# Kernel tuning notes

Hardware: AMD Instinct MI355X
Metric: run time of the kernel (lower is better)

## Reference

```python
import jax, jax.numpy as jnp
import numpy as np

B, S, D, H = 4, 2048, 1024, 16
HD = D // H  # 64


def setup_inputs() -> dict:
    key = jax.random.key(0)
    ks = jax.random.split(key, 4)
    scale = 0.02
    return {
        "hidden_states": jax.random.normal(ks[0], (B, S, D), dtype=jnp.float32),
        "pad": jnp.ones((B, S), dtype=jnp.float32),  # 1 = keep, 0 = pad
        "wq": jax.random.normal(ks[1], (D, D), dtype=jnp.float32) * scale,
        "bq": jnp.zeros((D,), dtype=jnp.float32),
        "wk": jax.random.normal(ks[2], (D, D), dtype=jnp.float32) * scale,
        "bk": jnp.zeros((D,), dtype=jnp.float32),
        "wv": jax.random.normal(ks[3], (D, D), dtype=jnp.float32) * scale,
        "bv": jnp.zeros((D,), dtype=jnp.float32),
    }


def reference(hidden_states, pad, wq, bq, wk, bk, wv, bv):
    # QKV projections (torch Linear: x @ W^T + b); weights stored as [out, in]
    q = hidden_states @ wq.T + bq  # [B,S,D]
    k = hidden_states @ wk.T + bk
    v = hidden_states @ wv.T + bv

    def split_heads(x):
        return x.reshape(B, S, H, HD).transpose(0, 2, 1, 3)  # [B,H,S,HD]

    q, k, v = split_heads(q), split_heads(k), split_heads(v)

    score = jnp.einsum("bhqd,bhkd->bhqk", q, k) / jnp.sqrt(jnp.float32(HD))
    # additive pad mask: (1 - pad) * -1e9, broadcast over heads and query dim
    mask_bias = (1.0 - pad)[:, None, None, :] * (-1e9)
    prob = jax.nn.softmax(score + mask_bias, axis=-1)  # [B,H,S,S]

    context = jnp.einsum("bhqk,bhkd->bhqd", prob, v)  # [B,H,S,HD]
    context = context.transpose(0, 2, 1, 3).reshape(B, S, D)
    return context
```

## Files before the change

kernel.cpp:

```cpp
#include <hip/hip_runtime.h>
#include <cstdint>
#include <cstddef>

#define B_ 4
#define S_ 2048
#define D_ 1024
#define H_ 16

typedef unsigned short u16;
typedef unsigned int u32;
typedef __attribute__((ext_vector_type(8))) short bf16x8;
typedef __attribute__((ext_vector_type(4))) float f32x4;

__device__ __forceinline__ u16 f2bf(float f) {
  union { float f; u32 u; } x; x.f = f;
  u32 r = x.u + 0x7fffu + ((x.u >> 16) & 1u);
  return (u16)(r >> 16);
}

__device__ __forceinline__ u32 cvtpk_bf16(float lo, float hi) {
  u32 r;
  asm("v_cvt_pk_bf16_f32 %0, %1, %2" : "=v"(r) : "v"(lo), "v"(hi));
  return r;
}

__device__ __forceinline__ float max3f(float a, float b, float c) {
  return fmaxf(fmaxf(a, b), c);
}

__device__ __forceinline__ f32x4 mfma16(bf16x8 a, bf16x8 b, f32x4 c) {
  return __builtin_amdgcn_mfma_f32_16x16x32_bf16(a, b, c, 0, 0, 0);
}

__device__ __forceinline__ void gload_lds16(const u16* g, u16* l) {
  __builtin_amdgcn_global_load_lds((const __attribute__((address_space(1))) void*)g,
                                   (__attribute__((address_space(3))) void*)l,
                                   16, 0, 0);
}

__global__ __launch_bounds__(256) void cvt_kernel(const float4* __restrict__ src,
                                                  uint2* __restrict__ dst, int n4) {
  int i = blockIdx.x * 256 + threadIdx.x;
  if (i < n4) {
    float4 v = src[i];
    uint2 o;
    o.x = cvtpk_bf16(v.x, v.y);
    o.y = cvtpk_bf16(v.z, v.w);
    dst[i] = o;
  }
}

__global__ __launch_bounds__(256) void qkv_gemm(
    const u16* __restrict__ A, const u16* __restrict__ Bm,
    const float* __restrict__ bq, const float* __restrict__ bk,
    const float* __restrict__ bv,
    u16* __restrict__ qbuf, u16* __restrict__ kbuf, u16* __restrict__ vtbuf)
{
  __shared__ __align__(16) u16 lA[128 * 64];
  __shared__ __align__(16) u16 lB[128 * 64];

  const int bid = blockIdx.x;
  const int wg = ((bid & 7) * 192) + (bid >> 3);
  const int bm = wg & 63;
  const int bn = wg >> 6;
  const int tid = threadIdx.x;
  const int wid = tid >> 6, lane = tid & 63;
  const int g = lane >> 4, c = lane & 15;
  const int wm = wid & 1, wn = wid >> 1;
  const int lrow = lane >> 3;
  const int lcb = (lane & 7) ^ lrow;

  f32x4 acc[4][4];
#pragma unroll
  for (int i = 0; i < 4; ++i)
#pragma unroll
    for (int j = 0; j < 4; ++j) acc[i][j] = (f32x4)0.0f;

  const u16* Ab = A + (size_t)(bm * 128) * 1024;
  const u16* Bb = Bm + (size_t)(bn * 128) * 1024;

  for (int kt = 0; kt < 16; ++kt) {
    const int k0 = kt * 64;
#pragma unroll
    for (int jj = 0; jj < 4; ++jj) {
      const int r0 = wid * 32 + jj * 8;
      gload_lds16(Ab + (size_t)(r0 + lrow) * 1024 + k0 + lcb * 8, lA + r0 * 64);
      gload_lds16(Bb + (size_t)(r0 + lrow) * 1024 + k0 + lcb * 8, lB + r0 * 64);
    }
    __syncthreads();
#pragma unroll
    for (int ks = 0; ks < 2; ++ks) {
      bf16x8 af[4], bfv[4];
#pragma unroll
      for (int mi = 0; mi < 4; ++mi) {
        const int row = wm * 64 + mi * 16 + c;
        const int cb = (ks * 4 + g) ^ (c & 7);
        af[mi] = *(const bf16x8*)(lA + row * 64 + cb * 8);
      }
#pragma unroll
      for (int ni = 0; ni < 4; ++ni) {
        const int row = wn * 64 + ni * 16 + c;
        const int cb = (ks * 4 + g) ^ (c & 7);
        bfv[ni] = *(const bf16x8*)(lB + row * 64 + cb * 8);
      }
#pragma unroll
      for (int mi = 0; mi < 4; ++mi)
#pragma unroll
        for (int ni = 0; ni < 4; ++ni)
          acc[mi][ni] = mfma16(af[mi], bfv[ni], acc[mi][ni]);
    }
    __syncthreads();
  }

  const int m0 = bm * 128 + wm * 64;
  const int n0 = bn * 128 + wn * 64;
#pragma unroll
  for (int ni = 0; ni < 4; ++ni) {
    const int col = n0 + ni * 16 + c;
    const int which = col >> 10;
    const int d = col & 1023;
    const int hh = d >> 6, hd = d & 63;
    const float* bp = (which == 0) ? bq : (which == 1) ? bk : bv;
    const float bias = bp[d];
#pragma unroll
    for (int mi = 0; mi < 4; ++mi) {
#pragma unroll
      for (int r = 0; r < 4; ++r) {
        const int row = m0 + mi * 16 + g * 4 + r;
        const int bb = row >> 11, ss = row & 2047;
        float val = acc[mi][ni][r] + bias;
        if (which == 0) {
          val *= 0.125f;
          qbuf[((size_t)(bb * 16 + hh) * 2048 + ss) * 64 + hd] = f2bf(val);
        } else if (which == 1) {
          kbuf[((size_t)(bb * 16 + hh) * 2048 + ss) * 64 + hd] = f2bf(val);
        } else {
          vtbuf[((size_t)(bb * 16 + hh) * 64 + hd) * 2048 + ss] = f2bf(val);
        }
      }
    }
  }
}

__global__ __launch_bounds__(256) void attn_kernel(
    const u16* __restrict__ qbuf, const u16* __restrict__ kbuf,
    const u16* __restrict__ vtbuf, const float* __restrict__ pad,
    float* __restrict__ out)
{
  __shared__ __align__(16) u16 lK[64 * 64];
  __shared__ __align__(16) u16 lV[64 * 64];
  __shared__ __align__(16) u16 lP[4 * 32 * 64];
  __shared__ __align__(16) float lMask[64];

  const int bid = blockIdx.x;
  const int wg = ((bid & 7) << 7) | (bid >> 3);
  const int bh = wg >> 4;
  const int qb = wg & 15;
  const int b = bh >> 4;
  const int h = bh & 15;
  const int tid = threadIdx.x;
  const int wid = tid >> 6, lane = tid & 63;
  const int g = lane >> 4, c = lane & 15;
  const int q0 = qb * 128 + wid * 32;

  const u16* qp = qbuf + (size_t)bh * S_ * 64;
  const u16* kp = kbuf + (size_t)bh * S_ * 64;
  const u16* vp = vtbuf + (size_t)bh * 64 * S_;

  bf16x8 qf[2][2];
#pragma unroll
  for (int nt = 0; nt < 2; ++nt)
#pragma unroll
    for (int ks = 0; ks < 2; ++ks)
      qf[nt][ks] = *(const bf16x8*)(qp + (size_t)(q0 + nt * 16 + c) * 64 + ks * 32 + g * 8);

  f32x4 o[2][4];
#pragma unroll
  for (int mi = 0; mi < 2; ++mi)
#pragma unroll
    for (int nh = 0; nh < 4; ++nh) o[mi][nh] = (f32x4)0.0f;

  float mst[2] = {-3e38f, -3e38f};
  float lst[2] = {0.0f, 0.0f};

  const int lrow = lane >> 3;
  const int lcb = (lane & 7) ^ lrow;
  u16* lPw = lP + wid * (32 * 64);
  const float LOG2E = 1.44269504f;

  for (int j = 0; j < 32; ++j) {
    const int kv0 = j * 64;
#pragma unroll
    for (int jj = 0; jj < 2; ++jj) {
      const int r0 = wid * 16 + jj * 8;
      gload_lds16(kp + (size_t)(kv0 + r0 + lrow) * 64 + lcb * 8, lK + r0 * 64);
      gload_lds16(vp + (size_t)(r0 + lrow) * 2048 + kv0 + lcb * 8, lV + r0 * 64);
    }
    if (tid < 64) lMask[tid] = (1.0f - pad[b * S_ + kv0 + tid]) * (-1e9f);
    __syncthreads();

    f32x4 st[4][2];
#pragma unroll
    for (int mt = 0; mt < 4; ++mt) { st[mt][0] = (f32x4)0.0f; st[mt][1] = (f32x4)0.0f; }
#pragma unroll
    for (int ks = 0; ks < 2; ++ks) {
#pragma unroll
      for (int mt = 0; mt < 4; ++mt) {
        const int row = mt * 16 + c;
        const int cb = (ks * 4 + g) ^ (c & 7);
        const bf16x8 kf = *(const bf16x8*)(lK + row * 64 + cb * 8);
        st[mt][0] = mfma16(kf, qf[0][ks], st[mt][0]);
        st[mt][1] = mfma16(kf, qf[1][ks], st[mt][1]);
      }
    }

    float mb[4][4];
#pragma unroll
    for (int mt = 0; mt < 4; ++mt) {
      const float4 m4 = *(const float4*)&lMask[mt * 16 + g * 4];
      mb[mt][0] = m4.x; mb[mt][1] = m4.y; mb[mt][2] = m4.z; mb[mt][3] = m4.w;
    }

#pragma unroll
    for (int nt = 0; nt < 2; ++nt) {
      float sv[16];
#pragma unroll
      for (int mt = 0; mt < 4; ++mt)
#pragma unroll
        for (int r = 0; r < 4; ++r) {
          const float v = st[mt][nt][r] + mb[mt][r];
          st[mt][nt][r] = v;
          sv[mt * 4 + r] = v;
        }
      float tmax = max3f(sv[0], sv[1], sv[2]);
      tmax = max3f(tmax, sv[3], sv[4]);
      tmax = max3f(tmax, sv[5], sv[6]);
      tmax = max3f(tmax, sv[7], sv[8]);
      tmax = max3f(tmax, sv[9], sv[10]);
      tmax = max3f(tmax, sv[11], sv[12]);
      tmax = max3f(tmax, sv[13], sv[14]);
      tmax = fmaxf(tmax, sv[15]);
      tmax = fmaxf(tmax, __shfl_xor(tmax, 16));
      tmax = fmaxf(tmax, __shfl_xor(tmax, 32));

      if (!__all(tmax - mst[nt] <= 8.0f)) {
        const float mnew = fmaxf(mst[nt], tmax);
        const float fac = exp2f((mst[nt] - mnew) * LOG2E);
        mst[nt] = mnew;
        lst[nt] *= fac;
#pragma unroll
        for (int r = 0; r < 4; ++r) {
          const float fr = __shfl(fac, g * 4 + r);
#pragma unroll
          for (int nh = 0; nh < 4; ++nh) o[nt][nh][r] *= fr;
        }
      }

      const float ml = mst[nt] * LOG2E;
      float rsum = 0.0f;
#pragma unroll
      for (int mt = 0; mt < 4; ++mt)
#pragma unroll
        for (int r = 0; r < 4; ++r) {
          const float p = exp2f(fmaf(st[mt][nt][r], LOG2E, -ml));
          st[mt][nt][r] = p;
          rsum += p;
        }
      rsum += __shfl_xor(rsum, 16);
      rsum += __shfl_xor(rsum, 32);
      lst[nt] += rsum;

#pragma unroll
      for (int mt = 0; mt < 4; ++mt) {
        uint2 pk;
        pk.x = cvtpk_bf16(st[mt][nt][0], st[mt][nt][1]);
        pk.y = cvtpk_bf16(st[mt][nt][2], st[mt][nt][3]);
        const int rowq = nt * 16 + c;
        const int cb = (2 * mt + (g >> 1)) ^ (c & 7);
        *(uint2*)(lPw + rowq * 64 + cb * 8 + (g & 1) * 4) = pk;
      }
    }

#pragma unroll
    for (int ks = 0; ks < 2; ++ks) {
      bf16x8 pa[2];
#pragma unroll
      for (int mi = 0; mi < 2; ++mi) {
        const int row = mi * 16 + c;
        const int cb = (ks * 4 + g) ^ (c & 7);
        pa[mi] = *(const bf16x8*)(lPw + row * 64 + cb * 8);
      }
#pragma unroll
      for (int nh = 0; nh < 4; ++nh) {
        const int row = nh * 16 + c;
        const int cb = (ks * 4 + g) ^ (c & 7);
        const bf16x8 vf = *(const bf16x8*)(lV + row * 64 + cb * 8);
#pragma unroll
        for (int mi = 0; mi < 2; ++mi)
          o[mi][nh] = mfma16(pa[mi], vf, o[mi][nh]);
      }
    }
    __syncthreads();
  }

#pragma unroll
  for (int mi = 0; mi < 2; ++mi) {
#pragma unroll
    for (int r = 0; r < 4; ++r) {
      const float lr = __shfl(lst[mi], g * 4 + r);
      const float inv = 1.0f / lr;
      const int srow = q0 + mi * 16 + g * 4 + r;
      float* op = out + (size_t)(b * S_ + srow) * D_ + h * 64;
#pragma unroll
      for (int nh = 0; nh < 4; ++nh)
        op[nh * 16 + c] = o[mi][nh][r] * inv;
    }
  }
}

extern "C" void kernel_launch(void* const* d_in, const int* in_sizes, int n_in,
                              void* d_out, int out_size, void* d_ws, size_t ws_size,
                              hipStream_t stream) {
  const float* hs  = (const float*)d_in[0];
  const float* pad = (const float*)d_in[1];
  const float* wq  = (const float*)d_in[2];
  const float* bq  = (const float*)d_in[3];
  const float* wk  = (const float*)d_in[4];
  const float* bk  = (const float*)d_in[5];
  const float* wv  = (const float*)d_in[6];
  const float* bv  = (const float*)d_in[7];
  float* out = (float*)d_out;

  char* ws = (char*)d_ws;
  u16* Abf   = (u16*)ws;
  u16* Bbf   = (u16*)(ws + (16u << 20));
  u16* qbuf  = (u16*)(ws + (22u << 20));
  u16* kbuf  = (u16*)(ws + (38u << 20));
  u16* vtbuf = (u16*)(ws + (54u << 20));

  cvt_kernel<<<8192, 256, 0, stream>>>((const float4*)hs, (uint2*)Abf, 2097152);
  cvt_kernel<<<1024, 256, 0, stream>>>((const float4*)wq, (uint2*)Bbf, 262144);
  cvt_kernel<<<1024, 256, 0, stream>>>((const float4*)wk, (uint2*)(Bbf + (1u << 20)), 262144);
  cvt_kernel<<<1024, 256, 0, stream>>>((const float4*)wv, (uint2*)(Bbf + (2u << 20)), 262144);

  qkv_gemm<<<1536, 256, 0, stream>>>(Abf, Bbf, bq, bk, bv, qbuf, kbuf, vtbuf);
  attn_kernel<<<1024, 256, 0, stream>>>(qbuf, kbuf, vtbuf, pad, out);
}
```

Baseline: 358.7 us.

## Rewrite QKV GEMM as 256x256 tile with 8-stage pipelined LDS and priority scheduling

Replaces the 128x128 single-buffered QKV projection GEMM with a 256x256 tile run by 512 threads. Operand loads go through an 8-slot circular LDS buffer (128 KB dynamic) with explicit vmcnt waits, barriers and setprio so that global-to-LDS copies overlap MFMA work. The goal is to hide memory latency and increase data reuse per tile. In exchange it uses much more LDS, which limits occupancy, and it adds fragile hand-scheduled synchronization.

```diff
diff --git a/kernel.cpp b/kernel.cpp
--- a/kernel.cpp
+++ b/kernel.cpp
@@ -50,85 +50,124 @@
   }
 }
 
-__global__ __launch_bounds__(256) void qkv_gemm(
+__global__ __launch_bounds__(512, 2) void qkv_gemm(
     const u16* __restrict__ A, const u16* __restrict__ Bm,
     const float* __restrict__ bq, const float* __restrict__ bk,
     const float* __restrict__ bv,
     u16* __restrict__ qbuf, u16* __restrict__ kbuf, u16* __restrict__ vtbuf)
 {
-  __shared__ __align__(16) u16 lA[128 * 64];
-  __shared__ __align__(16) u16 lB[128 * 64];
+  extern __shared__ __align__(16) u16 lds[];
 
   const int bid = blockIdx.x;
-  const int wg = ((bid & 7) * 192) + (bid >> 3);
-  const int bm = wg & 63;
-  const int bn = wg >> 6;
+  const int wg = (bid & 7) * 48 + (bid >> 3);
+  const int bm = wg & 31;
+  const int bn = wg >> 5;
   const int tid = threadIdx.x;
-  const int wid = tid >> 6, lane = tid & 63;
+  const int w = tid >> 6, lane = tid & 63;
   const int g = lane >> 4, c = lane & 15;
-  const int wm = wid & 1, wn = wid >> 1;
-  const int lrow = lane >> 3;
-  const int lcb = (lane & 7) ^ lrow;
-
-  f32x4 acc[4][4];
-#pragma unroll
-  for (int i = 0; i < 4; ++i)
+  const int wr = w >> 2, wc = w & 3;
+
+  const u16* Ab = A  + (size_t)(bm * 256) * 1024;
+  const u16* Bb = Bm + (size_t)(bn * 256) * 1024;
+
+  auto STAGE = [&](int h) {
+    const int T = h >> 2, q = h & 3, kh = q >> 1;
+    const u16* gp = (q & 1) ? Bb : Ab;
+    u16* sb = lds + (h & 7) * 8192;
+#pragma unroll
+    for (int j = 0; j < 2; ++j) {
+      const int blk = (w * 2 + j) * 64 + lane;
+      const int row = blk >> 2;
+      const int cb  = (blk & 3) ^ ((row >> 1) & 3);
+      gload_lds16(gp + (size_t)row * 1024 + T * 64 + kh * 32 + cb * 8,
+                  sb + (w * 2 + j) * 512);
+    }
+  };
+  auto LDA = [&](int slot, int m) -> bf16x8 {
+    const int row = wr * 128 + m * 16 + c;
+    const int blk = row * 4 + (g ^ ((row >> 1) & 3));
+    return *(const bf16x8*)(lds + slot * 8192 + blk * 8);
+  };
+  auto LDB = [&](int slot, int n) -> bf16x8 {
+    const int row = wc * 64 + n * 16 + c;
+    const int blk = row * 4 + (g ^ ((row >> 1) & 3));
+    return *(const bf16x8*)(lds + slot * 8192 + blk * 8);
+  };
+
+  f32x4 acc[8][4];
+#pragma unroll
+  for (int i = 0; i < 8; ++i)
 #pragma unroll
     for (int j = 0; j < 4; ++j) acc[i][j] = (f32x4)0.0f;
 
-  const u16* Ab = A + (size_t)(bm * 128) * 1024;
-  const u16* Bb = Bm + (size_t)(bn * 128) * 1024;
-
-  for (int kt = 0; kt < 16; ++kt) {
-    const int k0 = kt * 64;
-#pragma unroll
-    for (int jj = 0; jj < 4; ++jj) {
-      const int r0 = wid * 32 + jj * 8;
-      gload_lds16(Ab + (size_t)(r0 + lrow) * 1024 + k0 + lcb * 8, lA + r0 * 64);
-      gload_lds16(Bb + (size_t)(r0 + lrow) * 1024 + k0 + lcb * 8, lB + r0 * 64);
-    }
-    __syncthreads();
-#pragma unroll
-    for (int ks = 0; ks < 2; ++ks) {
-      bf16x8 af[4], bfv[4];
-#pragma unroll
-      for (int mi = 0; mi < 4; ++mi) {
-        const int row = wm * 64 + mi * 16 + c;
-        const int cb = (ks * 4 + g) ^ (c & 7);
-        af[mi] = *(const bf16x8*)(lA + row * 64 + cb * 8);
-      }
-#pragma unroll
-      for (int ni = 0; ni < 4; ++ni) {
-        const int row = wn * 64 + ni * 16 + c;
-        const int cb = (ks * 4 + g) ^ (c & 7);
-        bfv[ni] = *(const bf16x8*)(lB + row * 64 + cb * 8);
-      }
-#pragma unroll
-      for (int mi = 0; mi < 4; ++mi)
-#pragma unroll
-        for (int ni = 0; ni < 4; ++ni)
-          acc[mi][ni] = mfma16(af[mi], bfv[ni], acc[mi][ni]);
-    }
-    __syncthreads();
-  }
-
-  const int m0 = bm * 128 + wm * 64;
-  const int n0 = bn * 128 + wn * 64;
-#pragma unroll
-  for (int ni = 0; ni < 4; ++ni) {
-    const int col = n0 + ni * 16 + c;
-    const int which = col >> 10;
-    const int d = col & 1023;
+  bf16x8 a0, a1, a2, a3, b0, b1, b2, b3;
+
+#define MF4(ai, mi) \
+  acc[mi][0] = mfma16(ai, b0, acc[mi][0]); \
+  acc[mi][1] = mfma16(ai, b1, acc[mi][1]); \
+  acc[mi][2] = mfma16(ai, b2, acc[mi][2]); \
+  acc[mi][3] = mfma16(ai, b3, acc[mi][3]);
+
+#define VM6 asm volatile("s_waitcnt vmcnt(6)" ::: "memory");
+
+#define PHASE(SA, SB, MLO, STG, DOB, VM) \
+  a0 = LDA(SA, MLO + 0); a1 = LDA(SA, MLO + 1); \
+  a2 = LDA(SA, MLO + 2); a3 = LDA(SA, MLO + 3); \
+  if (DOB) { b0 = LDB(SB, 0); b1 = LDB(SB, 1); b2 = LDB(SB, 2); b3 = LDB(SB, 3); } \
+  STAGE(STG); \
+  __builtin_amdgcn_s_barrier(); \
+  asm volatile("s_waitcnt lgkmcnt(0)" ::: "memory"); \
+  __builtin_amdgcn_sched_barrier(0); \
+  __builtin_amdgcn_s_setprio(1); \
+  MF4(a0, MLO + 0) MF4(a1, MLO + 1) MF4(a2, MLO + 2) MF4(a3, MLO + 3) \
+  __builtin_amdgcn_s_setprio(0); \
+  VM \
+  __builtin_amdgcn_s_barrier();
+
+#define KTILE(S0, HB) \
+  PHASE(S0, S0 + 1, 0, HB + 0, 1, ) \
+  PHASE(S0, S0 + 1, 4, HB + 1, 0, VM6) \
+  PHASE(S0 + 2, S0 + 3, 0, HB + 2, 1, ) \
+  PHASE(S0 + 2, S0 + 3, 4, HB + 3, 0, VM6)
+
+  STAGE(0); STAGE(1); STAGE(2); STAGE(3); STAGE(4);
+  asm volatile("s_waitcnt vmcnt(6)" ::: "memory");
+  __builtin_amdgcn_s_barrier();
+
+  for (int tp = 0; tp < 7; ++tp) {
+    const int hb = 8 * tp + 5;
+    KTILE(0, hb)
+    KTILE(4, hb + 4)
+  }
+
+  STAGE(61); STAGE(62); STAGE(63);
+  asm volatile("s_waitcnt vmcnt(0)" ::: "memory");
+  __builtin_amdgcn_s_barrier();
+
+#define EPHASE(SA, SB, MLO, DOB) \
+  a0 = LDA(SA, MLO + 0); a1 = LDA(SA, MLO + 1); \
+  a2 = LDA(SA, MLO + 2); a3 = LDA(SA, MLO + 3); \
+  if (DOB) { b0 = LDB(SB, 0); b1 = LDB(SB, 1); b2 = LDB(SB, 2); b3 = LDB(SB, 3); } \
+  MF4(a0, MLO + 0) MF4(a1, MLO + 1) MF4(a2, MLO + 2) MF4(a3, MLO + 3)
+
+  EPHASE(0, 1, 0, 1) EPHASE(0, 1, 4, 0) EPHASE(2, 3, 0, 1) EPHASE(2, 3, 4, 0)
+  EPHASE(4, 5, 0, 1) EPHASE(4, 5, 4, 0) EPHASE(6, 7, 0, 1) EPHASE(6, 7, 4, 0)
+
+  const int which = bn >> 2;
+  const float* bp = (which == 0) ? bq : (which == 1) ? bk : bv;
+  const int m0r = bm * 256 + wr * 128;
+#pragma unroll
+  for (int n = 0; n < 4; ++n) {
+    const int d = (bn & 3) * 256 + wc * 64 + n * 16 + c;
     const int hh = d >> 6, hd = d & 63;
-    const float* bp = (which == 0) ? bq : (which == 1) ? bk : bv;
     const float bias = bp[d];
 #pragma unroll
-    for (int mi = 0; mi < 4; ++mi) {
+    for (int m = 0; m < 8; ++m) {
 #pragma unroll
       for (int r = 0; r < 4; ++r) {
-        const int row = m0 + mi * 16 + g * 4 + r;
+        const int row = m0r + m * 16 + g * 4 + r;
         const int bb = row >> 11, ss = row & 2047;
-        float val = acc[mi][ni][r] + bias;
+        float val = acc[m][n][r] + bias;
         if (which == 0) {
           val *= 0.125f;
           qbuf[((size_t)(bb * 16 + hh) * 2048 + ss) * 64 + hd] = f2bf(val);
@@ -140,6 +179,11 @@
       }
     }
   }
+#undef MF4
+#undef VM6
+#undef PHASE
+#undef KTILE
+#undef EPHASE
 }
 
 __global__ __launch_bounds__(256) void attn_kernel(
@@ -338,11 +382,14 @@
   u16* kbuf  = (u16*)(ws + (38u << 20));
   u16* vtbuf = (u16*)(ws + (54u << 20));
 
+  hipFuncSetAttribute(reinterpret_cast<const void*>(&qkv_gemm),
+                      hipFuncAttributeMaxDynamicSharedMemorySize, 131072);
+
   cvt_kernel<<<8192, 256, 0, stream>>>((const float4*)hs, (uint2*)Abf, 2097152);
   cvt_kernel<<<1024, 256, 0, stream>>>((const float4*)wq, (uint2*)Bbf, 262144);
   cvt_kernel<<<1024, 256, 0, stream>>>((const float4*)wk, (uint2*)(Bbf + (1u << 20)), 262144);
   cvt_kernel<<<1024, 256, 0, stream>>>((const float4*)wv, (uint2*)(Bbf + (2u << 20)), 262144);
 
-  qkv_gemm<<<1536, 256, 0, stream>>>(Abf, Bbf, bq, bk, bv, qbuf, kbuf, vtbuf);
+  qkv_gemm<<<384, 512, 131072, stream>>>(Abf, Bbf, bq, bk, bv, qbuf, kbuf, vtbuf);
   attn_kernel<<<1024, 256, 0, stream>>>(qbuf, kbuf, vtbuf, pad, out);
 }
```

New measurement: 367.0 us. 1.02x slower.
